# Kernel optimization log

Measured on AMD Instinct MI355X. Metric: run time of the kernel, lower is better.

The kernel has to match this reference:

```python
import jax, jax.numpy as jnp
import numpy as np

B, N = 1, 384          # batch, N_res
C_Z, C_H, H = 128, 32, 4  # pair channels, per-head hidden, heads
INF = 1.0e9
LN_EPS = 1e-5


def setup_inputs() -> dict:
    key = jax.random.key(0)
    ks = jax.random.split(key, 8)
    s = lambda k, shape: jax.random.normal(k, shape, jnp.float32) * 0.02
    return {
        "z": jax.random.normal(ks[0], (B, N, N, C_Z), jnp.float32),
        "mask": jnp.ones((B, N, N), jnp.float32),
        "ln_gamma": jnp.ones((C_Z,), jnp.float32),
        "ln_beta": jnp.zeros((C_Z,), jnp.float32),
        "w_bias": s(ks[1], (C_Z, H)),          # Linear(c_z, num_heads, bias=False)
        "w_q": s(ks[2], (C_Z, H * C_H)),        # no-bias q/k/v projections
        "w_k": s(ks[3], (C_Z, H * C_H)),
        "w_v": s(ks[4], (C_Z, H * C_H)),
        "w_g": s(ks[5], (C_Z, H * C_H)),        # gating projection
        "b_g": jnp.ones((H * C_H,), jnp.float32),  # gating bias init ones
        "w_o": s(ks[6], (H * C_H, C_Z)),        # output projection
        "b_o": jnp.zeros((C_Z,), jnp.float32),
    }


def reference(z, mask, ln_gamma, ln_beta, w_bias, w_q, w_k, w_v, w_g, b_g, w_o, b_o):
    # ta_type == "starting": no transposes.
    # LayerNorm over c_z
    mu = jnp.mean(z, axis=-1, keepdims=True)
    var = jnp.var(z, axis=-1, keepdims=True)
    zn = (z - mu) * jax.lax.rsqrt(var + LN_EPS) * ln_gamma + ln_beta  # [B,N,N,C_Z]

    # triangle bias: linear(z) -> [B,N,N,H] -> movedim -> [B,H,i,j], broadcast over batch-row axis
    tri_bias = jnp.einsum('bijc,ch->bhij', zn, w_bias)  # [B,H,N,N]
    # mask bias: masked keys get -inf; mask shape [B,i,k] broadcast to [B,i,1,1,k]
    mask_bias = INF * (mask - 1.0)

    wq = w_q.reshape(C_Z, H, C_H)
    wk = w_k.reshape(C_Z, H, C_H)
    wv = w_v.reshape(C_Z, H, C_H)
    q = jnp.einsum('bijc,chd->bijhd', zn, wq) * (C_H ** -0.5)  # scale q
    k = jnp.einsum('bijc,chd->bijhd', zn, wk)
    v = jnp.einsum('bijc,chd->bijhd', zn, wv)

    # attention over the j/k axis per row i: logits [B,i,H,j,k]
    logits = jnp.einsum('bijhd,bikhd->bihjk', q, k)
    logits = logits + mask_bias[:, :, None, None, :] + tri_bias[:, None, :, :, :]
    a = jax.nn.softmax(logits, axis=-1)
    o = jnp.einsum('bihjk,bikhd->bijhd', a, v)  # [B,N,N,H,C_H]

    # gating
    g = jax.nn.sigmoid(jnp.einsum('bijc,ce->bije', zn, w_g) + b_g)  # [B,N,N,H*C_H]
    o = o.reshape(B, N, N, H * C_H) * g
    return jnp.einsum('bije,ec->bijc', o, w_o) + b_o  # [B,N,N,C_Z]
```

## Files before the change

### kernel.cpp

```cpp
#include <hip/hip_runtime.h>

#define NRES 384
#define CZ 128
#define NH 4
#define CH 32
#define NN (NRES * NRES)
#define NNCZ ((size_t)NN * CZ)

typedef unsigned short u16;
typedef __attribute__((ext_vector_type(4))) unsigned short us4;
typedef __attribute__((ext_vector_type(8))) unsigned short us8;
typedef __attribute__((ext_vector_type(8))) short s8;
typedef __attribute__((ext_vector_type(4))) float f4;

__device__ __forceinline__ float bf2f(u16 u) {
  return __uint_as_float(((unsigned)u) << 16);
}
__device__ __forceinline__ u16 f2bf(float f) {
  unsigned u = __float_as_uint(f);
  u += 0x7fffu + ((u >> 16) & 1u);
  return (u16)(u >> 16);
}

template<bool F32>
__device__ __forceinline__ float ld1(const void* p, size_t i) {
  if constexpr (F32) return ((const float*)p)[i];
  else return bf2f(((const u16*)p)[i]);
}

template<bool F32>
__device__ __forceinline__ void ld4v(const void* p, size_t i, float o[4]) {
  if constexpr (F32) {
    const float4 a = *(const float4*)((const float*)p + i);
    o[0] = a.x; o[1] = a.y; o[2] = a.z; o[3] = a.w;
  } else {
    const us4 v = *(const us4*)((const u16*)p + i);
    #pragma unroll
    for (int u = 0; u < 4; ++u) o[u] = bf2f(v[u]);
  }
}

template<bool F32>
__device__ __forceinline__ void ld8(const void* p, size_t i, float o[8]) {
  if constexpr (F32) {
    const float4 a = *(const float4*)((const float*)p + i);
    const float4 b = *(const float4*)((const float*)p + i + 4);
    o[0] = a.x; o[1] = a.y; o[2] = a.z; o[3] = a.w;
    o[4] = b.x; o[5] = b.y; o[6] = b.z; o[7] = b.w;
  } else {
    const us8 v = *(const us8*)((const u16*)p + i);
    #pragma unroll
    for (int u = 0; u < 8; ++u) o[u] = bf2f(v[u]);
  }
}

__global__ void k_probe(const u16* __restrict__ z, int* __restrict__ flag) {
  int weird = 0;
  for (int i = threadIdx.x; i < 256; i += 64) {
    const int e = (z[i] >> 7) & 0xFF;
    if (e < 0x70 || e > 0x8F) weird++;
  }
  #pragma unroll
  for (int m = 1; m < 64; m <<= 1) weird += __shfl_xor(weird, m, 64);
  if (threadIdx.x == 0) *flag = (weird >= 16) ? 1 : 0;
}

template<bool F32>
__global__ void k_repack(const void* __restrict__ w0, const void* __restrict__ w1,
                         const void* __restrict__ w2, const void* __restrict__ w3,
                         const void* __restrict__ w4p, const void* __restrict__ w5b,
                         u16* __restrict__ dst, const int* __restrict__ flag) {
  if ((*flag != 0) != F32) return;
  const int a = blockIdx.x;
  u16* d = dst + (size_t)a * 16384;
  const int t = threadIdx.x;
  if (a == 5) {
    #pragma unroll
    for (int it = 0; it < 16; ++it) {
      const int c = (t >> 5) + it * 8;
      const int m0 = (t & 31) * 4;
      float w4[4] = {0.f, 0.f, 0.f, 0.f};
      if (m0 == 0) ld4v<F32>(w5b, (size_t)c * NH, w4);
      const int ks = c >> 5, qq = (c >> 3) & 3, j = c & 7;
      #pragma unroll
      for (int mm = 0; mm < 4; ++mm) {
        const int m = m0 + mm;
        d[ks * 4096 + (((m >> 4) * 4 + qq) * 16 + (m & 15)) * 8 + j] = f2bf(w4[mm]);
      }
    }
    return;
  }
  const void* W = (a == 0) ? w0 : (a == 1) ? w1 : (a == 2) ? w2 : (a == 3) ? w3 : w4p;
  const float scl = (a == 0) ? 0.17677669529663687f : 1.0f;
  #pragma unroll
  for (int it = 0; it < 16; ++it) {
    const int c = (t >> 5) + it * 8;
    const int m0 = (t & 31) * 4;
    float w4[4];
    ld4v<F32>(W, (size_t)c * CZ + m0, w4);
    const int ks = c >> 5, qq = (c >> 3) & 3, j = c & 7;
    #pragma unroll
    for (int mm = 0; mm < 4; ++mm) {
      const int m = m0 + mm;
      d[ks * 4096 + (((m >> 4) * 4 + qq) * 16 + (m & 15)) * 8 + j] = f2bf(w4[mm] * scl);
    }
  }
}

template<bool F32>
__global__ __launch_bounds__(256, 2) void k_ln_proj(
    const void* __restrict__ z, const void* __restrict__ gma, const void* __restrict__ bta,
    const u16* __restrict__ wrep, const void* __restrict__ bg,
    u16* __restrict__ qb, u16* __restrict__ kb, u16* __restrict__ vb, u16* __restrict__ gb,
    float* __restrict__ triT, const int* __restrict__ flag)
{
  if ((*flag != 0) != F32) return;
  __shared__ __align__(16) u16 znl[128 * 136];
  const int t = threadIdx.x;
  const int lane = t & 63;
  const int wid = t >> 6;
  const int n16 = lane & 15;
  const int quad = lane >> 4;
  const int rowBase = blockIdx.x * 128;

  const int c0 = n16 * 8;
  float g8[8], b8[8];
  ld8<F32>(gma, c0, g8);
  ld8<F32>(bta, c0, b8);
  for (int it = 0; it < 8; ++it) {
    const int rl = wid * 32 + it * 4 + quad;
    float x[8];
    ld8<F32>(z, (size_t)(rowBase + rl) * CZ + c0, x);
    float s = 0.f, q2 = 0.f;
    #pragma unroll
    for (int u = 0; u < 8; ++u) { s += x[u]; q2 += x[u] * x[u]; }
    #pragma unroll
    for (int m = 1; m < 16; m <<= 1) {
      s  += __shfl_xor(s, m, 64);
      q2 += __shfl_xor(q2, m, 64);
    }
    const float mu = s * (1.0f / CZ);
    const float rs = rsqrtf(q2 * (1.0f / CZ) - mu * mu + 1e-5f);
    us8 o;
    #pragma unroll
    for (int u = 0; u < 8; ++u) o[u] = f2bf((x[u] - mu) * rs * g8[u] + b8[u]);
    *(us8*)&znl[rl * 136 + c0] = o;
  }
  __syncthreads();

  {
    const u16* WTb = wrep + (size_t)5 * 16384;
    f4 acc2[2];
    acc2[0] = f4{0.f, 0.f, 0.f, 0.f};
    acc2[1] = f4{0.f, 0.f, 0.f, 0.f};
    #pragma unroll
    for (int ks = 0; ks < 4; ++ks) {
      const s8 ab = *(const s8*)&WTb[ks * 4096 + (quad * 16 + n16) * 8];
      #pragma unroll
      for (int i = 0; i < 2; ++i) {
        const s8 b = *(const s8*)&znl[((wid * 2 + i) * 16 + n16) * 136 + ks * 32 + quad * 8];
        acc2[i] = __builtin_amdgcn_mfma_f32_16x16x32_bf16(ab, b, acc2[i], 0, 0, 0);
      }
    }
    if (quad == 0) {
      #pragma unroll
      for (int i = 0; i < 2; ++i) {
        const int P = rowBase + (wid * 2 + i) * 16 + n16;
        const int aI = P / NRES, bI = P % NRES;
        #pragma unroll
        for (int r = 0; r < 4; ++r)
          triT[(size_t)r * NN + (size_t)bI * NRES + aI] = acc2[i][r];
      }
    }
  }

  for (int arr = 0; arr < 4; ++arr) {
    const u16* WTg = wrep + (size_t)arr * 16384;

    f4 acc[2][8];
    #pragma unroll
    for (int i = 0; i < 2; ++i)
      #pragma unroll
      for (int nt = 0; nt < 8; ++nt) acc[i][nt] = f4{0.f, 0.f, 0.f, 0.f};

    #pragma unroll
    for (int ks = 0; ks < 4; ++ks) {
      s8 a[2], b[8];
      #pragma unroll
      for (int i = 0; i < 2; ++i)
        a[i] = *(const s8*)&WTg[ks * 4096 + (((wid * 2 + i) * 4 + quad) * 16 + n16) * 8];
      #pragma unroll
      for (int nt = 0; nt < 8; ++nt)
        b[nt] = *(const s8*)&znl[(nt * 16 + n16) * 136 + ks * 32 + quad * 8];
      #pragma unroll
      for (int i = 0; i < 2; ++i)
        #pragma unroll
        for (int nt = 0; nt < 8; ++nt)
          acc[i][nt] = __builtin_amdgcn_mfma_f32_16x16x32_bf16(a[i], b[nt], acc[i][nt], 0, 0, 0);
    }

    u16* dstb = (arr == 0) ? qb : (arr == 1) ? kb : (arr == 2) ? vb : gb;
    #pragma unroll
    for (int i = 0; i < 2; ++i) {
      const int mt = wid * 2 + i;
      const int och0 = mt * 16 + quad * 4;
      float e4[4];
      if (arr == 3) ld4v<F32>(bg, och0, e4);
      #pragma unroll
      for (int nt = 0; nt < 8; ++nt) {
        us4 o;
        #pragma unroll
        for (int r = 0; r < 4; ++r) {
          float v = acc[i][nt][r];
          if (arr == 3) v = 1.0f / (1.0f + __expf(-(v + e4[r])));
          o[r] = f2bf(v);
        }
        *(us4*)&dstb[(size_t)(rowBase + nt * 16 + n16) * CZ + och0] = o;
      }
    }
  }
}

template<bool F32>
__global__ __launch_bounds__(256, 3) void k_attn(
    const u16* __restrict__ qb, const u16* __restrict__ kb, const u16* __restrict__ vb,
    const u16* __restrict__ gb, const float* __restrict__ triT, const void* __restrict__ msk,
    u16* __restrict__ ogb, const int* __restrict__ flag)
{
  if ((*flag != 0) != F32) return;
  __shared__ __align__(16) u16 VB[12 * 4 * 32 * 8];
  __shared__ __align__(16) u16 Pch[4][2][16 * 40];
  __shared__ __align__(16) float mbL[NRES];
  const int t = threadIdx.x;
  const int i = blockIdx.x >> 2;
  const int h = blockIdx.x & 3;
  const size_t base_i = (size_t)i * NRES;

  #pragma unroll
  for (int it = 0; it < 12; ++it) {
    const int idx = t + it * 256;
    const int kk = idx >> 3;
    const int d0 = (idx & 7) * 4;
    const us4 vv = *(const us4*)&vb[(base_i + kk) * CZ + h * CH + d0];
    const int cc2 = kk >> 5;
    const int kap = kk & 31;
    const int p = 2 * (kap & 15) + (kap >> 4);
    u16* vdst = &VB[((cc2 * 4 + (p >> 3)) * 32 + d0) * 8 + (p & 7)];
    vdst[0] = vv[0]; vdst[8] = vv[1]; vdst[16] = vv[2]; vdst[24] = vv[3];
  }
  for (int idx = t; idx < NRES; idx += 256)
    mbL[idx] = 1.0e9f * (ld1<F32>(msk, base_i + idx) - 1.0f);
  __syncthreads();

  const int wid = t >> 6;
  const int lane = t & 63;
  const int n = lane & 15;
  const int quad = lane >> 4;
  const float* trih = triT + (size_t)h * NN;
  u16* pbA = &Pch[wid][0][0];
  u16* pbB = &Pch[wid][1][0];

  for (int pr = wid; pr < 12; pr += 4) {
    const int jrowA = pr * 32;
    const int jrowB = jrowA + 16;
    const s8 aqA = *(const s8*)&qb[(base_i + jrowA + n) * CZ + h * CH + quad * 8];
    const s8 aqB = *(const s8*)&qb[(base_i + jrowB + n) * CZ + h * CH + quad * 8];

    f4 O0A = {0.f,0.f,0.f,0.f}, O1A = {0.f,0.f,0.f,0.f};
    f4 O0B = {0.f,0.f,0.f,0.f}, O1B = {0.f,0.f,0.f,0.f};
    f4 lA = {0.f,0.f,0.f,0.f}, lB = {0.f,0.f,0.f,0.f};
    f4 mA = {-1.0e30f,-1.0e30f,-1.0e30f,-1.0e30f};
    f4 mB = {-1.0e30f,-1.0e30f,-1.0e30f,-1.0e30f};

    s8 bk[4];
    #pragma unroll
    for (int u = 0; u < 4; ++u)
      bk[u] = *(const s8*)&kb[(base_i + u * 16 + n) * CZ + h * CH + quad * 8];

    #pragma unroll 1
    for (int cc = 0; cc < 6; ++cc) {
      f4 SA[4], SB[4];
      #pragma unroll
      for (int u = 0; u < 4; ++u) {
        const f4 z4 = {0.f, 0.f, 0.f, 0.f};
        SA[u] = __builtin_amdgcn_mfma_f32_16x16x32_bf16(aqA, bk[u], z4, 0, 0, 0);
        SB[u] = __builtin_amdgcn_mfma_f32_16x16x32_bf16(aqB, bk[u], z4, 0, 0, 0);
      }
      if (cc < 5) {
        #pragma unroll
        for (int u = 0; u < 4; ++u)
          bk[u] = *(const s8*)&kb[(base_i + ((cc + 1) * 4 + u) * 16 + n) * CZ + h * CH + quad * 8];
      }
      #pragma unroll
      for (int u = 0; u < 4; ++u) {
        const int tt = cc * 4 + u;
        const float mbv = mbL[tt * 16 + n];
        const size_t trow = (size_t)(tt * 16 + n) * NRES;
        const float4 tA = *(const float4*)&trih[trow + jrowA + quad * 4];
        const float4 tB = *(const float4*)&trih[trow + jrowB + quad * 4];
        SA[u][0] += tA.x + mbv; SA[u][1] += tA.y + mbv;
        SA[u][2] += tA.z + mbv; SA[u][3] += tA.w + mbv;
        SB[u][0] += tB.x + mbv; SB[u][1] += tB.y + mbv;
        SB[u][2] += tB.z + mbv; SB[u][3] += tB.w + mbv;
      }
      f4 mxA = SA[0], mxB = SB[0];
      #pragma unroll
      for (int u = 1; u < 4; ++u) {
        #pragma unroll
        for (int r = 0; r < 4; ++r) {
          mxA[r] = fmaxf(mxA[r], SA[u][r]);
          mxB[r] = fmaxf(mxB[r], SB[u][r]);
        }
      }
      #pragma unroll
      for (int sft = 1; sft < 16; sft <<= 1) {
        #pragma unroll
        for (int r = 0; r < 4; ++r) {
          mxA[r] = fmaxf(mxA[r], __shfl_xor(mxA[r], sft, 64));
          mxB[r] = fmaxf(mxB[r], __shfl_xor(mxB[r], sft, 64));
        }
      }
      #pragma unroll
      for (int r = 0; r < 4; ++r) {
        const float mnA = fmaxf(mA[r], mxA[r]);
        const float scA = __expf(mA[r] - mnA);
        mA[r] = mnA;
        O0A[r] *= scA; O1A[r] *= scA; lA[r] *= scA;
        const float mnB = fmaxf(mB[r], mxB[r]);
        const float scB = __expf(mB[r] - mnB);
        mB[r] = mnB;
        O0B[r] *= scB; O1B[r] *= scB; lB[r] *= scB;
      }
      #pragma unroll
      for (int u = 0; u < 4; ++u) {
        #pragma unroll
        for (int r = 0; r < 4; ++r) {
          SA[u][r] = __expf(SA[u][r] - mA[r]);
          lA[r] += SA[u][r];
          SB[u][r] = __expf(SB[u][r] - mB[r]);
          lB[r] += SB[u][r];
        }
      }
      #pragma unroll
      for (int s = 0; s < 2; ++s) {
        #pragma unroll
        for (int r = 0; r < 4; ++r) {
          const unsigned wA = (unsigned)f2bf(SA[2 * s][r]) |
                              ((unsigned)f2bf(SA[2 * s + 1][r]) << 16);
          *(unsigned*)&pbA[(quad * 4 + r) * 40 + n * 2] = wA;
          const unsigned wB = (unsigned)f2bf(SB[2 * s][r]) |
                              ((unsigned)f2bf(SB[2 * s + 1][r]) << 16);
          *(unsigned*)&pbB[(quad * 4 + r) * 40 + n * 2] = wB;
        }
        const int C = cc * 2 + s;
        const s8 apA = *(const s8*)&pbA[n * 40 + quad * 8];
        const s8 apB = *(const s8*)&pbB[n * 40 + quad * 8];
        const s8 bv0 = *(const s8*)&VB[((C * 4 + quad) * 32 + n) * 8];
        const s8 bv1 = *(const s8*)&VB[((C * 4 + quad) * 32 + 16 + n) * 8];
        O0A = __builtin_amdgcn_mfma_f32_16x16x32_bf16(apA, bv0, O0A, 0, 0, 0);
        O1A = __builtin_amdgcn_mfma_f32_16x16x32_bf16(apA, bv1, O1A, 0, 0, 0);
        O0B = __builtin_amdgcn_mfma_f32_16x16x32_bf16(apB, bv0, O0B, 0, 0, 0);
        O1B = __builtin_amdgcn_mfma_f32_16x16x32_bf16(apB, bv1, O1B, 0, 0, 0);
      }
    }

    f4 sA = lA, sB = lB;
    #pragma unroll
    for (int sft = 1; sft < 16; sft <<= 1) {
      #pragma unroll
      for (int r = 0; r < 4; ++r) {
        sA[r] += __shfl_xor(sA[r], sft, 64);
        sB[r] += __shfl_xor(sB[r], sft, 64);
      }
    }
    #pragma unroll
    for (int r = 0; r < 4; ++r) {
      const float ivA = 1.0f / sA[r];
      const size_t rowA = (base_i + jrowA + quad * 4 + r) * CZ + h * CH;
      const float gA0 = bf2f(gb[rowA + n]);
      const float gA1 = bf2f(gb[rowA + 16 + n]);
      ogb[rowA + n]      = f2bf(O0A[r] * ivA * gA0);
      ogb[rowA + 16 + n] = f2bf(O1A[r] * ivA * gA1);
      const float ivB = 1.0f / sB[r];
      const size_t rowB = (base_i + jrowB + quad * 4 + r) * CZ + h * CH;
      const float gB0 = bf2f(gb[rowB + n]);
      const float gB1 = bf2f(gb[rowB + 16 + n]);
      ogb[rowB + n]      = f2bf(O0B[r] * ivB * gB0);
      ogb[rowB + 16 + n] = f2bf(O1B[r] * ivB * gB1);
    }
  }
}

template<bool F32>
__global__ __launch_bounds__(256, 2) void k_out(
    const u16* __restrict__ og, const u16* __restrict__ wrep, const void* __restrict__ bo,
    void* __restrict__ outp, const int* __restrict__ flag)
{
  if ((*flag != 0) != F32) return;
  __shared__ __align__(16) u16 ol[128 * 136];
  const u16* WTg = wrep + (size_t)4 * 16384;
  const int t = threadIdx.x;
  const int lane = t & 63;
  const int wid = t >> 6;
  const int n16 = lane & 15;
  const int quad = lane >> 4;
  const int rowBase = blockIdx.x * 128;

  #pragma unroll
  for (int it = 0; it < 8; ++it) {
    const int idx8 = t + it * 256;
    const int r = idx8 >> 4;
    const int c0 = (idx8 & 15) * 8;
    *(us8*)&ol[r * 136 + c0] = *(const us8*)&og[(size_t)(rowBase + r) * CZ + c0];
  }
  __syncthreads();

  f4 acc[2][8];
  #pragma unroll
  for (int i = 0; i < 2; ++i)
    #pragma unroll
    for (int nt = 0; nt < 8; ++nt) acc[i][nt] = f4{0.f, 0.f, 0.f, 0.f};

  #pragma unroll
  for (int ks = 0; ks < 4; ++ks) {
    s8 a[2], b[8];
    #pragma unroll
    for (int i = 0; i < 2; ++i)
      a[i] = *(const s8*)&WTg[ks * 4096 + (((wid * 2 + i) * 4 + quad) * 16 + n16) * 8];
    #pragma unroll
    for (int nt = 0; nt < 8; ++nt)
      b[nt] = *(const s8*)&ol[(nt * 16 + n16) * 136 + ks * 32 + quad * 8];
    #pragma unroll
    for (int i = 0; i < 2; ++i)
      #pragma unroll
      for (int nt = 0; nt < 8; ++nt)
        acc[i][nt] = __builtin_amdgcn_mfma_f32_16x16x32_bf16(a[i], b[nt], acc[i][nt], 0, 0, 0);
  }

  #pragma unroll
  for (int i = 0; i < 2; ++i) {
    const int och0 = (wid * 2 + i) * 16 + quad * 4;
    float b4[4];
    ld4v<F32>(bo, och0, b4);
    #pragma unroll
    for (int nt = 0; nt < 8; ++nt) {
      const size_t off = (size_t)(rowBase + nt * 16 + n16) * CZ + och0;
      if constexpr (F32) {
        float4 o;
        o.x = acc[i][nt][0] + b4[0]; o.y = acc[i][nt][1] + b4[1];
        o.z = acc[i][nt][2] + b4[2]; o.w = acc[i][nt][3] + b4[3];
        *(float4*)&((float*)outp)[off] = o;
      } else {
        us4 o;
        #pragma unroll
        for (int r = 0; r < 4; ++r) o[r] = f2bf(acc[i][nt][r] + b4[r]);
        *(us4*)&((u16*)outp)[off] = o;
      }
    }
  }
}

extern "C" void kernel_launch(void* const* d_in, const int* in_sizes, int n_in,
                              void* d_out, int out_size, void* d_ws, size_t ws_size,
                              hipStream_t stream) {
  const void* z     = d_in[0];
  const void* msk   = d_in[1];
  const void* gma   = d_in[2];
  const void* bta   = d_in[3];
  const void* wbias = d_in[4];
  const void* wq    = d_in[5];
  const void* wk    = d_in[6];
  const void* wv    = d_in[7];
  const void* wg    = d_in[8];
  const void* bg    = d_in[9];
  const void* wo    = d_in[10];
  const void* bo    = d_in[11];

  char* ws = (char*)d_ws;
  int* flag = (int*)ws;
  u16* qb = (u16*)(ws + 256);
  u16* kb = qb + NNCZ;
  u16* vb = kb + NNCZ;
  u16* gb = vb + NNCZ;
  float* triT = (float*)(gb + NNCZ);
  u16* wrep = (u16*)(triT + (size_t)NH * NN);
  u16* ogb = qb;

  k_probe<<<dim3(1), dim3(64), 0, stream>>>((const u16*)z, flag);

  k_repack<false><<<dim3(6), dim3(256), 0, stream>>>(wq, wk, wv, wg, wo, wbias, wrep, flag);
  k_repack<true><<<dim3(6), dim3(256), 0, stream>>>(wq, wk, wv, wg, wo, wbias, wrep, flag);

  k_ln_proj<false><<<dim3(NN / 128), dim3(256), 0, stream>>>(
      z, gma, bta, wrep, bg, qb, kb, vb, gb, triT, flag);
  k_ln_proj<true><<<dim3(NN / 128), dim3(256), 0, stream>>>(
      z, gma, bta, wrep, bg, qb, kb, vb, gb, triT, flag);

  k_attn<false><<<dim3(NRES * NH), dim3(256), 0, stream>>>(
      qb, kb, vb, gb, triT, msk, ogb, flag);
  k_attn<true><<<dim3(NRES * NH), dim3(256), 0, stream>>>(
      qb, kb, vb, gb, triT, msk, ogb, flag);

  k_out<false><<<dim3(NN / 128), dim3(256), 0, stream>>>(ogb, wrep, bo, d_out, flag);
  k_out<true><<<dim3(NN / 128), dim3(256), 0, stream>>>(ogb, wrep, bo, d_out, flag);
}
```

Measured before the change: 437.9 us.

## Transpose QK^T MFMA so softmax rows live per lane, drop LDS P staging

Swaps the MFMA operands for the logits so each lane holds a query row across key columns. This shrinks the row max and sum reductions from 4-step shuffles over 16 lanes to two cross-quad shuffles. The probability tile is now packed to bf16 and rearranged into the PV operand with register shuffles, replacing the per-wave LDS round-trip. To match, the V LDS layout drops its interleave, and the triangle-bias buffer is stored un-transposed so bias loads are contiguous along k. The cost is many more ds_bpermute shuffles and per-row rescale broadcasts.

Result: faster. 422.4 us (-3.5%).

```diff
diff --git a/kernel.cpp b/kernel.cpp
--- a/kernel.cpp
+++ b/kernel.cpp
@@ -12,6 +12,7 @@
 typedef __attribute__((ext_vector_type(8))) unsigned short us8;
 typedef __attribute__((ext_vector_type(8))) short s8;
 typedef __attribute__((ext_vector_type(4))) float f4;
+typedef __attribute__((ext_vector_type(4))) unsigned ui4;
 
 __device__ __forceinline__ float bf2f(u16 u) {
   return __uint_as_float(((unsigned)u) << 16);
@@ -20,6 +21,9 @@
   unsigned u = __float_as_uint(f);
   u += 0x7fffu + ((u >> 16) & 1u);
   return (u16)(u >> 16);
+}
+__device__ __forceinline__ unsigned pk2(float lo, float hi) {
+  return (unsigned)f2bf(lo) | ((unsigned)f2bf(hi) << 16);
 }
 
 template<bool F32>
@@ -169,7 +173,7 @@
         const int aI = P / NRES, bI = P % NRES;
         #pragma unroll
         for (int r = 0; r < 4; ++r)
-          triT[(size_t)r * NN + (size_t)bI * NRES + aI] = acc2[i][r];
+          triT[(size_t)r * NN + (size_t)aI * NRES + bI] = acc2[i][r];
       }
     }
   }
@@ -229,7 +233,6 @@
 {
   if ((*flag != 0) != F32) return;
   __shared__ __align__(16) u16 VB[12 * 4 * 32 * 8];
-  __shared__ __align__(16) u16 Pch[4][2][16 * 40];
   __shared__ __align__(16) float mbL[NRES];
   const int t = threadIdx.x;
   const int i = blockIdx.x >> 2;
@@ -244,8 +247,7 @@
     const us4 vv = *(const us4*)&vb[(base_i + kk) * CZ + h * CH + d0];
     const int cc2 = kk >> 5;
     const int kap = kk & 31;
-    const int p = 2 * (kap & 15) + (kap >> 4);
-    u16* vdst = &VB[((cc2 * 4 + (p >> 3)) * 32 + d0) * 8 + (p & 7)];
+    u16* vdst = &VB[((cc2 * 4 + (kap >> 3)) * 32 + d0) * 8 + (kap & 7)];
     vdst[0] = vv[0]; vdst[8] = vv[1]; vdst[16] = vv[2]; vdst[24] = vv[3];
   }
   for (int idx = t; idx < NRES; idx += 256)
@@ -257,8 +259,9 @@
   const int n = lane & 15;
   const int quad = lane >> 4;
   const float* trih = triT + (size_t)h * NN;
-  u16* pbA = &Pch[wid][0][0];
-  u16* pbB = &Pch[wid][1][0];
+  const int src0 = n + ((quad & 1) << 5);
+  const int src1 = src0 + 16;
+  const bool hiq = quad >= 2;
 
   for (int pr = wid; pr < 12; pr += 4) {
     const int jrowA = pr * 32;
@@ -268,9 +271,8 @@
 
     f4 O0A = {0.f,0.f,0.f,0.f}, O1A = {0.f,0.f,0.f,0.f};
     f4 O0B = {0.f,0.f,0.f,0.f}, O1B = {0.f,0.f,0.f,0.f};
-    f4 lA = {0.f,0.f,0.f,0.f}, lB = {0.f,0.f,0.f,0.f};
-    f4 mA = {-1.0e30f,-1.0e30f,-1.0e30f,-1.0e30f};
-    f4 mB = {-1.0e30f,-1.0e30f,-1.0e30f,-1.0e30f};
+    float lA = 0.f, lB = 0.f;
+    float mA = -1.0e30f, mB = -1.0e30f;
 
     s8 bk[4];
     #pragma unroll
@@ -283,8 +285,8 @@
       #pragma unroll
       for (int u = 0; u < 4; ++u) {
         const f4 z4 = {0.f, 0.f, 0.f, 0.f};
-        SA[u] = __builtin_amdgcn_mfma_f32_16x16x32_bf16(aqA, bk[u], z4, 0, 0, 0);
-        SB[u] = __builtin_amdgcn_mfma_f32_16x16x32_bf16(aqB, bk[u], z4, 0, 0, 0);
+        SA[u] = __builtin_amdgcn_mfma_f32_16x16x32_bf16(bk[u], aqA, z4, 0, 0, 0);
+        SB[u] = __builtin_amdgcn_mfma_f32_16x16x32_bf16(bk[u], aqB, z4, 0, 0, 0);
       }
       if (cc < 5) {
         #pragma unroll
@@ -293,95 +295,99 @@
       }
       #pragma unroll
       for (int u = 0; u < 4; ++u) {
-        const int tt = cc * 4 + u;
-        const float mbv = mbL[tt * 16 + n];
-        const size_t trow = (size_t)(tt * 16 + n) * NRES;
-        const float4 tA = *(const float4*)&trih[trow + jrowA + quad * 4];
-        const float4 tB = *(const float4*)&trih[trow + jrowB + quad * 4];
-        SA[u][0] += tA.x + mbv; SA[u][1] += tA.y + mbv;
-        SA[u][2] += tA.z + mbv; SA[u][3] += tA.w + mbv;
-        SB[u][0] += tB.x + mbv; SB[u][1] += tB.y + mbv;
-        SB[u][2] += tB.z + mbv; SB[u][3] += tB.w + mbv;
-      }
-      f4 mxA = SA[0], mxB = SB[0];
+        const int kb0 = (cc * 4 + u) * 16 + quad * 4;
+        const float4 mb4 = *(const float4*)&mbL[kb0];
+        const float4 tA = *(const float4*)&trih[(size_t)(jrowA + n) * NRES + kb0];
+        const float4 tB = *(const float4*)&trih[(size_t)(jrowB + n) * NRES + kb0];
+        SA[u][0] += tA.x + mb4.x; SA[u][1] += tA.y + mb4.y;
+        SA[u][2] += tA.z + mb4.z; SA[u][3] += tA.w + mb4.w;
+        SB[u][0] += tB.x + mb4.x; SB[u][1] += tB.y + mb4.y;
+        SB[u][2] += tB.z + mb4.z; SB[u][3] += tB.w + mb4.w;
+      }
+      float mxA = fmaxf(fmaxf(SA[0][0], SA[0][1]), fmaxf(SA[0][2], SA[0][3]));
+      float mxB = fmaxf(fmaxf(SB[0][0], SB[0][1]), fmaxf(SB[0][2], SB[0][3]));
       #pragma unroll
       for (int u = 1; u < 4; ++u) {
-        #pragma unroll
-        for (int r = 0; r < 4; ++r) {
-          mxA[r] = fmaxf(mxA[r], SA[u][r]);
-          mxB[r] = fmaxf(mxB[r], SB[u][r]);
-        }
-      }
-      #pragma unroll
-      for (int sft = 1; sft < 16; sft <<= 1) {
-        #pragma unroll
-        for (int r = 0; r < 4; ++r) {
-          mxA[r] = fmaxf(mxA[r], __shfl_xor(mxA[r], sft, 64));
-          mxB[r] = fmaxf(mxB[r], __shfl_xor(mxB[r], sft, 64));
-        }
-      }
+        mxA = fmaxf(mxA, fmaxf(fmaxf(SA[u][0], SA[u][1]), fmaxf(SA[u][2], SA[u][3])));
+        mxB = fmaxf(mxB, fmaxf(fmaxf(SB[u][0], SB[u][1]), fmaxf(SB[u][2], SB[u][3])));
+      }
+      mxA = fmaxf(mxA, __shfl_xor(mxA, 16, 64));
+      mxA = fmaxf(mxA, __shfl_xor(mxA, 32, 64));
+      mxB = fmaxf(mxB, __shfl_xor(mxB, 16, 64));
+      mxB = fmaxf(mxB, __shfl_xor(mxB, 32, 64));
+      const float mnA = fmaxf(mA, mxA);
+      const float scA = __expf(mA - mnA);
+      mA = mnA; lA *= scA;
+      const float mnB = fmaxf(mB, mxB);
+      const float scB = __expf(mB - mnB);
+      mB = mnB; lB *= scB;
       #pragma unroll
       for (int r = 0; r < 4; ++r) {
-        const float mnA = fmaxf(mA[r], mxA[r]);
-        const float scA = __expf(mA[r] - mnA);
-        mA[r] = mnA;
-        O0A[r] *= scA; O1A[r] *= scA; lA[r] *= scA;
-        const float mnB = fmaxf(mB[r], mxB[r]);
-        const float scB = __expf(mB[r] - mnB);
-        mB[r] = mnB;
-        O0B[r] *= scB; O1B[r] *= scB; lB[r] *= scB;
+        const float srA = __shfl(scA, quad * 4 + r, 16);
+        O0A[r] *= srA; O1A[r] *= srA;
+        const float srB = __shfl(scB, quad * 4 + r, 16);
+        O0B[r] *= srB; O1B[r] *= srB;
       }
       #pragma unroll
       for (int u = 0; u < 4; ++u) {
         #pragma unroll
         for (int r = 0; r < 4; ++r) {
-          SA[u][r] = __expf(SA[u][r] - mA[r]);
-          lA[r] += SA[u][r];
-          SB[u][r] = __expf(SB[u][r] - mB[r]);
-          lB[r] += SB[u][r];
+          SA[u][r] = __expf(SA[u][r] - mA);
+          lA += SA[u][r];
+          SB[u][r] = __expf(SB[u][r] - mB);
+          lB += SB[u][r];
         }
       }
       #pragma unroll
       for (int s = 0; s < 2; ++s) {
-        #pragma unroll
-        for (int r = 0; r < 4; ++r) {
-          const unsigned wA = (unsigned)f2bf(SA[2 * s][r]) |
-                              ((unsigned)f2bf(SA[2 * s + 1][r]) << 16);
-          *(unsigned*)&pbA[(quad * 4 + r) * 40 + n * 2] = wA;
-          const unsigned wB = (unsigned)f2bf(SB[2 * s][r]) |
-                              ((unsigned)f2bf(SB[2 * s + 1][r]) << 16);
-          *(unsigned*)&pbB[(quad * 4 + r) * 40 + n * 2] = wB;
-        }
         const int C = cc * 2 + s;
-        const s8 apA = *(const s8*)&pbA[n * 40 + quad * 8];
-        const s8 apB = *(const s8*)&pbB[n * 40 + quad * 8];
         const s8 bv0 = *(const s8*)&VB[((C * 4 + quad) * 32 + n) * 8];
         const s8 bv1 = *(const s8*)&VB[((C * 4 + quad) * 32 + 16 + n) * 8];
-        O0A = __builtin_amdgcn_mfma_f32_16x16x32_bf16(apA, bv0, O0A, 0, 0, 0);
-        O1A = __builtin_amdgcn_mfma_f32_16x16x32_bf16(apA, bv1, O1A, 0, 0, 0);
-        O0B = __builtin_amdgcn_mfma_f32_16x16x32_bf16(apB, bv0, O0B, 0, 0, 0);
-        O1B = __builtin_amdgcn_mfma_f32_16x16x32_bf16(apB, bv1, O1B, 0, 0, 0);
-      }
-    }
-
-    f4 sA = lA, sB = lB;
-    #pragma unroll
-    for (int sft = 1; sft < 16; sft <<= 1) {
-      #pragma unroll
-      for (int r = 0; r < 4; ++r) {
-        sA[r] += __shfl_xor(sA[r], sft, 64);
-        sB[r] += __shfl_xor(sB[r], sft, 64);
-      }
-    }
+        {
+          const unsigned lo0 = pk2(SA[2*s][0], SA[2*s][1]);
+          const unsigned lo1 = pk2(SA[2*s][2], SA[2*s][3]);
+          const unsigned hi0 = pk2(SA[2*s+1][0], SA[2*s+1][1]);
+          const unsigned hi1 = pk2(SA[2*s+1][2], SA[2*s+1][3]);
+          const unsigned x0l = __shfl(lo0, src0, 64), x0h = __shfl(hi0, src0, 64);
+          const unsigned x1l = __shfl(lo1, src0, 64), x1h = __shfl(hi1, src0, 64);
+          const unsigned x2l = __shfl(lo0, src1, 64), x2h = __shfl(hi0, src1, 64);
+          const unsigned x3l = __shfl(lo1, src1, 64), x3h = __shfl(hi1, src1, 64);
+          const ui4 W = { hiq ? x0h : x0l, hiq ? x1h : x1l,
+                          hiq ? x2h : x2l, hiq ? x3h : x3l };
+          const s8 apA = __builtin_bit_cast(s8, W);
+          O0A = __builtin_amdgcn_mfma_f32_16x16x32_bf16(apA, bv0, O0A, 0, 0, 0);
+          O1A = __builtin_amdgcn_mfma_f32_16x16x32_bf16(apA, bv1, O1A, 0, 0, 0);
+        }
+        {
+          const unsigned lo0 = pk2(SB[2*s][0], SB[2*s][1]);
+          const unsigned lo1 = pk2(SB[2*s][2], SB[2*s][3]);
+          const unsigned hi0 = pk2(SB[2*s+1][0], SB[2*s+1][1]);
+          const unsigned hi1 = pk2(SB[2*s+1][2], SB[2*s+1][3]);
+          const unsigned x0l = __shfl(lo0, src0, 64), x0h = __shfl(hi0, src0, 64);
+          const unsigned x1l = __shfl(lo1, src0, 64), x1h = __shfl(hi1, src0, 64);
+          const unsigned x2l = __shfl(lo0, src1, 64), x2h = __shfl(hi0, src1, 64);
+          const unsigned x3l = __shfl(lo1, src1, 64), x3h = __shfl(hi1, src1, 64);
+          const ui4 W = { hiq ? x0h : x0l, hiq ? x1h : x1l,
+                          hiq ? x2h : x2l, hiq ? x3h : x3l };
+          const s8 apB = __builtin_bit_cast(s8, W);
+          O0B = __builtin_amdgcn_mfma_f32_16x16x32_bf16(apB, bv0, O0B, 0, 0, 0);
+          O1B = __builtin_amdgcn_mfma_f32_16x16x32_bf16(apB, bv1, O1B, 0, 0, 0);
+        }
+      }
+    }
+
+    float sA = lA, sB = lB;
+    sA += __shfl_xor(sA, 16, 64); sA += __shfl_xor(sA, 32, 64);
+    sB += __shfl_xor(sB, 16, 64); sB += __shfl_xor(sB, 32, 64);
     #pragma unroll
     for (int r = 0; r < 4; ++r) {
-      const float ivA = 1.0f / sA[r];
+      const float ivA = 1.0f / __shfl(sA, quad * 4 + r, 16);
       const size_t rowA = (base_i + jrowA + quad * 4 + r) * CZ + h * CH;
       const float gA0 = bf2f(gb[rowA + n]);
       const float gA1 = bf2f(gb[rowA + 16 + n]);
       ogb[rowA + n]      = f2bf(O0A[r] * ivA * gA0);
       ogb[rowA + 16 + n] = f2bf(O1A[r] * ivA * gA1);
-      const float ivB = 1.0f / sB[r];
+      const float ivB = 1.0f / __shfl(sB, quad * 4 + r, 16);
       const size_t rowB = (base_i + jrowB + quad * 4 + r) * CZ + h * CH;
       const float gB0 = bf2f(gb[rowB + n]);
       const float gB1 = bf2f(gb[rowB + 16 + n]);
```
